# Performance work log

Measured on AMD Instinct MI355X. Metric: run time of the kernel, lower is better.

The kernel has to match this reference:

```python
import jax, jax.numpy as jnp
import numpy as np

B, CIN, IMG, PATCH = 4, 1, 64, 8
SIDE = IMG // PATCH            # 8
N = SIDE ** 3                  # 512 tokens
C = 384
HEADS, HD = 6, 64
IFF = 1536
WS, SHIFT = 2, 1
NB = 4                         # 4 dense blocks + 4 shifted-window blocks (8 layers)
NKP = 15
EPS = 1e-5


def _ln(x, g, b):
    m = x.mean(-1, keepdims=True)
    v = ((x - m) ** 2).mean(-1, keepdims=True)
    return (x - m) * jax.lax.rsqrt(v + EPS) * g + b


def _mhsa(x, qw, kw, vw, pw, pb):
    # per-head Q/K/V linears (no bias), stacked as [H, C, HD]
    q = jnp.einsum('bnc,hcd->bhnd', x, qw)
    k = jnp.einsum('bnc,hcd->bhnd', x, kw)
    v = jnp.einsum('bnc,hcd->bhnd', x, vw)
    a = jax.nn.softmax(jnp.einsum('bhnd,bhmd->bhnm', q, k) / np.float32(np.sqrt(HD)), axis=-1)
    o = jnp.einsum('bhnm,bhmd->bhnd', a, v)
    o = o.transpose(0, 2, 1, 3).reshape(x.shape[0], x.shape[1], C)
    return o @ pw + pb


def _swin_attn(x, qkv_w, qkv_b, pw, pb):
    Bn = x.shape[0]
    H = W = D = SIDE
    xv = x.transpose(0, 2, 1).reshape(Bn, C, H, W, D)
    xv = jnp.roll(xv, (-SHIFT, -SHIFT, -SHIFT), axis=(2, 3, 4))
    # window partition -> [Bn*nw^3, WS^3, C]
    xv = xv.reshape(Bn, C, H // WS, WS, W // WS, WS, D // WS, WS)
    win = xv.transpose(0, 2, 4, 6, 3, 5, 7, 1).reshape(-1, WS ** 3, C)
    qkv = win @ qkv_w + qkv_b                                      # [Bw, ws3, 3C]
    qkv = qkv.reshape(win.shape[0], WS ** 3, 3, HEADS, HD).transpose(2, 0, 3, 1, 4)
    q, k, v = qkv[0], qkv[1], qkv[2]
    a = jax.nn.softmax(jnp.einsum('whnd,whmd->whnm', q, k) / np.float32(np.sqrt(HD)), axis=-1)
    o = jnp.einsum('whnm,whmd->whnd', a, v)
    o = o.transpose(0, 2, 1, 3).reshape(win.shape[0], WS ** 3, C)
    o = o @ pw + pb
    # window reverse
    o = o.reshape(Bn, H // WS, W // WS, D // WS, WS, WS, WS, C)
    o = o.transpose(0, 7, 1, 4, 2, 5, 3, 6).reshape(Bn, C, H, W, D)
    o = jnp.roll(o, (SHIFT, SHIFT, SHIFT), axis=(2, 3, 4))
    return o.reshape(Bn, C, -1).transpose(0, 2, 1)


def _ffn(x, w1, b1, w2, b2):
    return jax.nn.relu(x @ w1 + b1) @ w2 + b2


def _deconv2(x, w, b):
    # ConvTranspose3d kernel=stride=2 (no overlap): pure block upsample GEMM
    Bn, Cc, H, W, D = x.shape
    O = w.shape[1]
    y = jnp.einsum('bchwd,coijk->bohiwjdk', x, w)
    return y.reshape(Bn, O, 2 * H, 2 * W, 2 * D) + b[None, :, None, None, None]


def _bn_relu(x, g, b, m, v):
    sh = (1, -1, 1, 1, 1)
    y = (x - m.reshape(sh)) * jax.lax.rsqrt(v.reshape(sh) + EPS) * g.reshape(sh) + b.reshape(sh)
    return jax.nn.relu(y)


def setup_inputs() -> dict:
    key = jax.random.key(0)
    ks = iter(jax.random.split(key, 40))
    nrm = lambda shape, s=0.02: jax.random.normal(next(ks), shape, jnp.float32) * s
    inp = {
        'x': jax.random.normal(next(ks), (B, CIN, IMG, IMG, IMG), jnp.float32),
        'patch_w': nrm((C, CIN, PATCH, PATCH, PATCH)),
        'patch_b': jnp.zeros((C,), jnp.float32),
        'pos_emb': nrm((1, N, C)),
        # 4 dense blocks (stacked)
        'm_ln1_g': jnp.ones((NB, C)), 'm_ln1_b': jnp.zeros((NB, C)),
        'm_qw': nrm((NB, HEADS, C, HD)), 'm_kw': nrm((NB, HEADS, C, HD)), 'm_vw': nrm((NB, HEADS, C, HD)),
        'm_proj_w': nrm((NB, C, C)), 'm_proj_b': jnp.zeros((NB, C)),
        'm_ln2_g': jnp.ones((NB, C)), 'm_ln2_b': jnp.zeros((NB, C)),
        'm_w1': nrm((NB, C, IFF)), 'm_b1': jnp.zeros((NB, IFF)),
        'm_w2': nrm((NB, IFF, C)), 'm_b2': jnp.zeros((NB, C)),
        # 4 shifted-window blocks (stacked)
        's_ln1_g': jnp.ones((NB, C)), 's_ln1_b': jnp.zeros((NB, C)),
        's_qkv_w': nrm((NB, C, 3 * C)), 's_qkv_b': jnp.zeros((NB, 3 * C)),
        's_proj_w': nrm((NB, C, C)), 's_proj_b': jnp.zeros((NB, C)),
        's_ln2_g': jnp.ones((NB, C)), 's_ln2_b': jnp.zeros((NB, C)),
        's_w1': nrm((NB, C, IFF)), 's_b1': jnp.zeros((NB, IFF)),
        's_w2': nrm((NB, IFF, C)), 's_b2': jnp.zeros((NB, C)),
        # ClassicDecoder
        'd1_w': nrm((C, C, 2, 2, 2)), 'd1_b': jnp.zeros((C,)),
        'bn1_g': jnp.ones((C,)), 'bn1_b': jnp.zeros((C,)), 'bn1_m': jnp.zeros((C,)), 'bn1_v': jnp.ones((C,)),
        'd2_w': nrm((C, C, 2, 2, 2)), 'd2_b': jnp.zeros((C,)),
        'bn2_g': jnp.ones((C,)), 'bn2_b': jnp.zeros((C,)), 'bn2_m': jnp.zeros((C,)), 'bn2_v': jnp.ones((C,)),
        'out_w': nrm((NKP, C)), 'out_b': jnp.zeros((NKP,)),
    }
    return inp


def reference(x, patch_w, patch_b, pos_emb,
              m_ln1_g, m_ln1_b, m_qw, m_kw, m_vw, m_proj_w, m_proj_b,
              m_ln2_g, m_ln2_b, m_w1, m_b1, m_w2, m_b2,
              s_ln1_g, s_ln1_b, s_qkv_w, s_qkv_b, s_proj_w, s_proj_b,
              s_ln2_g, s_ln2_b, s_w1, s_b1, s_w2, s_b2,
              d1_w, d1_b, bn1_g, bn1_b, bn1_m, bn1_v,
              d2_w, d2_b, bn2_g, bn2_b, bn2_m, bn2_v,
              out_w, out_b):
    # patch embedding: Conv3d(k=stride=patch) -> [B, N, C]
    t = jax.lax.conv_general_dilated(x, patch_w, (PATCH, PATCH, PATCH), 'VALID',
                                     dimension_numbers=('NCDHW', 'OIDHW', 'NCDHW'))
    t = t + patch_b[None, :, None, None, None]
    t = t.reshape(B, C, N).transpose(0, 2, 1) + pos_emb
    for i in range(2 * NB):
        j = i // 2
        if i % 2 == 0:  # dense Block
            t = t + _mhsa(_ln(t, m_ln1_g[j], m_ln1_b[j]), m_qw[j], m_kw[j], m_vw[j], m_proj_w[j], m_proj_b[j])
            t = t + _ffn(_ln(t, m_ln2_g[j], m_ln2_b[j]), m_w1[j], m_b1[j], m_w2[j], m_b2[j])
        else:           # ShiftedWindowBlock
            t = t + _swin_attn(_ln(t, s_ln1_g[j], s_ln1_b[j]), s_qkv_w[j], s_qkv_b[j], s_proj_w[j], s_proj_b[j])
            t = t + _ffn(_ln(t, s_ln2_g[j], s_ln2_b[j]), s_w1[j], s_b1[j], s_w2[j], s_b2[j])
    # ClassicDecoder
    y = t.transpose(0, 2, 1).reshape(B, C, SIDE, SIDE, SIDE)
    y = _bn_relu(_deconv2(y, d1_w, d1_b), bn1_g, bn1_b, bn1_m, bn1_v)
    y = _bn_relu(_deconv2(y, d2_w, d2_b), bn2_g, bn2_b, bn2_m, bn2_v)
    y = jnp.einsum('bchwd,oc->bohwd', y, out_w) + out_b[None, :, None, None, None]
    return y
```

## Files before the change

### kernel.cpp

```cpp
#include <hip/hip_runtime.h>
#include <hip/hip_bf16.h>


typedef unsigned short u16;
typedef __bf16 bf16x8 __attribute__((ext_vector_type(8)));
typedef unsigned short u16x8 __attribute__((ext_vector_type(8)));
typedef float f32x4 __attribute__((ext_vector_type(4)));

__device__ __forceinline__ u16 f2bf(float f) {
  unsigned u = __builtin_bit_cast(unsigned, f);
  return (u16)((u + 0x7FFFu + ((u >> 16) & 1u)) >> 16);
}
__device__ __forceinline__ float bf2f(u16 b) {
  unsigned u = ((unsigned)b) << 16;
  return __builtin_bit_cast(float, u);
}

#define GLOAD_LDS16(g, l)                                                      \
  __builtin_amdgcn_global_load_lds(                                            \
      (const __attribute__((address_space(1))) unsigned int*)(const void*)(g), \
      (__attribute__((address_space(3))) unsigned int*)(void*)(l), 16, 0, 0)

struct MmP {
  const u16* A;
  const u16* Bt;
  const float* bias;
  void* C;
  void* aux;
  const float* e1; const float* e2; const float* e3; const float* e4;
  int K, ZH, lda, ldb, ldc;
  long aSb, aSh, bSb, bSh, cSb, cSh;
};

template<int MODE, int BM>
__global__ __launch_bounds__(256) void mfma_gemm(MmP p) {
  const int z = blockIdx.z;
  const int zb = z / p.ZH, zh = z - zb * p.ZH;
  const u16* A  = p.A  + zb * p.aSb + zh * p.aSh;
  const u16* Bt = p.Bt + zb * p.bSb + zh * p.bSh;
  const int m0 = blockIdx.y * BM, n0 = blockIdx.x * 64;

  __shared__ u16 As[2][BM * 64];
  __shared__ u16 Bs[2][64 * 64];

  const int tid = threadIdx.x;
  const int wid = tid >> 6, lane = tid & 63;
  constexpr int MI = BM / 32;
  const int wm = (wid >> 1) * (BM / 2), wn = (wid & 1) * 32;
  const int lr = lane & 15, lg = lane >> 4;
  constexpr int ACH = BM / 32;

  f32x4 acc[MI][2];
  #pragma unroll
  for (int i = 0; i < MI; i++)
    #pragma unroll
    for (int j = 0; j < 2; j++) acc[i][j] = (f32x4){0.f, 0.f, 0.f, 0.f};

  auto stage = [&](int buf, int kt) {
    #pragma unroll
    for (int i = 0; i < ACH; i++) {
      int c = i * 256 + tid;
      int row = c >> 3, cc = c & 7;
      int gk = ((cc ^ (row & 7)) << 3) + (kt << 6);
      GLOAD_LDS16(A + (long)(m0 + row) * p.lda + gk, As[buf] + c * 8);
    }
    #pragma unroll
    for (int i = 0; i < 2; i++) {
      int c = i * 256 + tid;
      int row = c >> 3, cc = c & 7;
      int gk = ((cc ^ (row & 7)) << 3) + (kt << 6);
      GLOAD_LDS16(Bt + (long)(n0 + row) * p.ldb + gk, Bs[buf] + c * 8);
    }
  };

  const int nKT = p.K >> 6;
  stage(0, 0);
  asm volatile("s_waitcnt vmcnt(0)");
  __syncthreads();

  int cur = 0;
  for (int kt = 0; kt < nKT; ++kt) {
    const bool more = (kt + 1 < nKT);
    if (more) stage(cur ^ 1, kt + 1);

    bf16x8 af[MI][2], bfr[2][2];
    #pragma unroll
    for (int i = 0; i < MI; i++)
      #pragma unroll
      for (int ks = 0; ks < 2; ks++) {
        int row = wm + i * 16 + lr;
        int j = ks * 4 + lg;
        af[i][ks] = *(const bf16x8*)(As[cur] + (row * 8 + (j ^ (row & 7))) * 8);
      }
    #pragma unroll
    for (int jn = 0; jn < 2; jn++)
      #pragma unroll
      for (int ks = 0; ks < 2; ks++) {
        int row = wn + jn * 16 + lr;
        int j = ks * 4 + lg;
        bfr[jn][ks] = *(const bf16x8*)(Bs[cur] + (row * 8 + (j ^ (row & 7))) * 8);
      }
    #pragma unroll
    for (int i = 0; i < MI; i++)
      #pragma unroll
      for (int jn = 0; jn < 2; jn++)
        #pragma unroll
        for (int ks = 0; ks < 2; ks++)
          acc[i][jn] = __builtin_amdgcn_mfma_f32_16x16x32_bf16(
              af[i][ks], bfr[jn][ks], acc[i][jn], 0, 0, 0);

    if (more) {
      asm volatile("s_waitcnt vmcnt(0)");
      __syncthreads();
      cur ^= 1;
    }
  }

  const long coff = zb * p.cSb + zh * p.cSh;
  #pragma unroll
  for (int i = 0; i < MI; i++) {
    const int rowb = m0 + wm + i * 16 + lg * 4;
    #pragma unroll
    for (int jn = 0; jn < 2; jn++) {
      const int col = n0 + wn + jn * 16 + lr;
      const float bv = p.bias ? p.bias[col] : 0.f;
      #pragma unroll
      for (int r = 0; r < 4; r++) {
        const int row = rowb + r;
        const float v = acc[i][jn][r];
        if constexpr (MODE == 0) {
          ((u16*)p.C)[coff + (long)row * p.ldc + col] = f2bf(v + bv);
        } else if constexpr (MODE == 1) {
          ((float*)p.C)[coff + (long)row * p.ldc + col] =
              v + bv + p.e1[(long)(row & 511) * 384 + col];
        } else if constexpr (MODE == 2) {
          ((float*)p.C)[coff + (long)row * p.ldc + col] += v + bv;
        } else if constexpr (MODE == 3) {
          ((u16*)p.C)[coff + (long)row * p.ldc + col] = f2bf(fmaxf(v + bv, 0.f));
        } else if constexpr (MODE == 5) {
          float raw = v + bv;
          float val = fmaxf((raw - p.e3[col]) * rsqrtf(p.e4[col] + 1e-5f) * p.e1[col] + p.e2[col], 0.f);
          int b = row >> 9, hwd = row & 511;
          int h = hwd >> 6, w = (hwd >> 3) & 7, d = hwd & 7;
          int i_ = zh >> 2, j_ = (zh >> 1) & 1, k_ = zh & 1;
          long tokn = (long)b * 4096 + (2 * h + i_) * 256 + (2 * w + j_) * 16 + (2 * d + k_);
          ((u16*)p.C)[tokn * 384 + col] = f2bf(val);
        } else if constexpr (MODE == 7) {
          u16 bv16 = f2bf(v);
          ((u16*)p.C)[coff + (long)row * p.ldc + col] = bv16;
          if (col >= 768) {
            int bb = row >> 9, tt = row & 511;
            int hh = (col - 768) >> 6, dd = col & 63;
            ((u16*)p.aux)[(((long)bb * 6 + hh) << 15) + (dd << 9) + tt] = bv16;
          }
        }
      }
    }
  }
}

__global__ __launch_bounds__(512) void dc2_k(const u16* __restrict__ y1, const u16* __restrict__ wd2,
                                             const float* __restrict__ d2b,
                                             const float* __restrict__ g, const float* __restrict__ bta,
                                             const float* __restrict__ mu, const float* __restrict__ var,
                                             const u16* __restrict__ owT, const float* __restrict__ ob,
                                             float* __restrict__ out) {
  __shared__ char smem[114688];
  u16* As = (u16*)smem;
  u16* Bs = (u16*)(smem + 16384);
  u16* H2 = (u16*)(smem + 16384);

  const int ijk = blockIdx.y;
  const int m0 = blockIdx.x * 64;
  const u16* Bt = wd2 + (long)ijk * 147456;
  const int tid = threadIdx.x;
  const int wid = tid >> 6, lane = tid & 63;
  const int wr = wid >> 2, wc = wid & 3;
  const int lr = lane & 15, lg = lane >> 4;

  f32x4 acc[2][6];
  #pragma unroll
  for (int i = 0; i < 2; i++)
    #pragma unroll
    for (int j = 0; j < 6; j++) acc[i][j] = (f32x4){0.f, 0.f, 0.f, 0.f};

  auto stage = [&](int buf, int kt) {
    {
      int c = tid;
      int row = c >> 3, cc = c & 7;
      int gk = ((cc ^ (row & 7)) << 3) + (kt << 6);
      GLOAD_LDS16(y1 + (long)(m0 + row) * 384 + gk, As + buf * 4096 + c * 8);
    }
    #pragma unroll
    for (int i = 0; i < 6; i++) {
      int c = i * 512 + tid;
      int row = c >> 3, cc = c & 7;
      int gk = ((cc ^ (row & 7)) << 3) + (kt << 6);
      GLOAD_LDS16(Bt + (long)row * 384 + gk, Bs + buf * 24576 + c * 8);
    }
  };
  stage(0, 0);
  asm volatile("s_waitcnt vmcnt(0)");
  __syncthreads();
  int cur = 0;
  for (int kt = 0; kt < 6; ++kt) {
    const bool more = (kt < 5);
    if (more) stage(cur ^ 1, kt + 1);
    bf16x8 af[2][2], bfr[6][2];
    #pragma unroll
    for (int i = 0; i < 2; i++)
      #pragma unroll
      for (int ks = 0; ks < 2; ks++) {
        int row = wr * 32 + i * 16 + lr;
        int j = ks * 4 + lg;
        af[i][ks] = *(const bf16x8*)(As + cur * 4096 + (row * 8 + (j ^ (row & 7))) * 8);
      }
    #pragma unroll
    for (int jn = 0; jn < 6; jn++)
      #pragma unroll
      for (int ks = 0; ks < 2; ks++) {
        int row = wc * 96 + jn * 16 + lr;
        int j = ks * 4 + lg;
        bfr[jn][ks] = *(const bf16x8*)(Bs + cur * 24576 + (row * 8 + (j ^ (row & 7))) * 8);
      }
    #pragma unroll
    for (int i = 0; i < 2; i++)
      #pragma unroll
      for (int jn = 0; jn < 6; jn++)
        #pragma unroll
        for (int ks = 0; ks < 2; ks++)
          acc[i][jn] = __builtin_amdgcn_mfma_f32_16x16x32_bf16(
              af[i][ks], bfr[jn][ks], acc[i][jn], 0, 0, 0);
    if (more) {
      asm volatile("s_waitcnt vmcnt(0)");
      __syncthreads();
      cur ^= 1;
    }
  }
  __syncthreads();

  #pragma unroll
  for (int i = 0; i < 2; i++)
    #pragma unroll
    for (int jn = 0; jn < 6; jn++) {
      const int col = wc * 96 + jn * 16 + lr;
      const float scale = rsqrtf(var[col] + 1e-5f) * g[col];
      const float bias2 = bta[col] - mu[col] * scale;
      const float db = d2b[col];
      #pragma unroll
      for (int r = 0; r < 4; r++) {
        int row = wr * 32 + i * 16 + lg * 4 + r;
        float val = fmaxf((acc[i][jn][r] + db) * scale + bias2, 0.f);
        H2[row * 392 + col] = f2bf(val);
      }
    }
  __syncthreads();

  if (wid < 4) {
    f32x4 c4 = (f32x4){0.f, 0.f, 0.f, 0.f};
    #pragma unroll
    for (int mf = 0; mf < 12; mf++) {
      bf16x8 af = *(const bf16x8*)(H2 + (wid * 16 + lr) * 392 + mf * 32 + lg * 8);
      bf16x8 bf = *(const bf16x8*)(owT + lr * 384 + mf * 32 + lg * 8);
      c4 = __builtin_amdgcn_mfma_f32_16x16x32_bf16(af, bf, c4, 0, 0, 0);
    }
    if (lr < 15) {
      const int i_ = ijk >> 2, j_ = (ijk >> 1) & 1, k_ = ijk & 1;
      const float bkp = ob[lr];
      #pragma unroll
      for (int r = 0; r < 4; r++) {
        const int gm = m0 + wid * 16 + lg * 4 + r;
        const int b = gm >> 12, h = (gm >> 8) & 15, w = (gm >> 4) & 15, d = gm & 15;
        const long o = ((long)(b * 15 + lr) << 15) + (2 * h + i_) * 1024 + (2 * w + j_) * 32 + (2 * d + k_);
        out[o] = c4[r] + bkp;
      }
    }
  }
}

__global__ __launch_bounds__(256) void attnsm_k(const u16* __restrict__ qkv, u16* __restrict__ P) {
  const int bh = blockIdx.y;
  const int b = bh / 6, h = bh - b * 6;
  const int qt = blockIdx.x;
  const int tid = threadIdx.x, wid = tid >> 6, lane = tid & 63;
  const int lr = lane & 15, lg = lane >> 4;
  __shared__ u16 Ks[512 * 64];
  const u16* qbase = qkv + ((long)b * 512) * 1152 + h * 64;

  #pragma unroll
  for (int i = 0; i < 16; i++) {
    int c = i * 256 + tid;
    int t = c >> 3, cc = c & 7;
    int gk = (cc ^ (t & 7)) << 3;
    GLOAD_LDS16(qbase + (long)t * 1152 + 384 + gk, Ks + c * 8);
  }
  const int qrow = qt * 64 + wid * 16 + lr;
  bf16x8 qf[2];
  #pragma unroll
  for (int ks = 0; ks < 2; ks++)
    qf[ks] = *(const bf16x8*)(qbase + (long)qrow * 1152 + (ks * 4 + lg) * 8);
  asm volatile("s_waitcnt vmcnt(0)");
  __syncthreads();

  f32x4 s[32];
  #pragma unroll
  for (int nt = 0; nt < 32; nt++) {
    s[nt] = (f32x4){0.f, 0.f, 0.f, 0.f};
    #pragma unroll
    for (int ks = 0; ks < 2; ks++) {
      int row = nt * 16 + lr;
      int j = ks * 4 + lg;
      bf16x8 kf = *(const bf16x8*)(Ks + (row * 8 + (j ^ (row & 7))) * 8);
      s[nt] = __builtin_amdgcn_mfma_f32_16x16x32_bf16(qf[ks], kf, s[nt], 0, 0, 0);
    }
  }
  float mx[4] = {-1e30f, -1e30f, -1e30f, -1e30f};
  #pragma unroll
  for (int nt = 0; nt < 32; nt++)
    #pragma unroll
    for (int r = 0; r < 4; r++) { s[nt][r] *= 0.125f; mx[r] = fmaxf(mx[r], s[nt][r]); }
  #pragma unroll
  for (int o = 8; o >= 1; o >>= 1)
    #pragma unroll
    for (int r = 0; r < 4; r++) mx[r] = fmaxf(mx[r], __shfl_xor(mx[r], o));
  float sum[4] = {0.f, 0.f, 0.f, 0.f};
  #pragma unroll
  for (int nt = 0; nt < 32; nt++)
    #pragma unroll
    for (int r = 0; r < 4; r++) { float e = __expf(s[nt][r] - mx[r]); s[nt][r] = e; sum[r] += e; }
  #pragma unroll
  for (int o = 8; o >= 1; o >>= 1)
    #pragma unroll
    for (int r = 0; r < 4; r++) sum[r] += __shfl_xor(sum[r], o);
  float inv[4];
  #pragma unroll
  for (int r = 0; r < 4; r++) inv[r] = 1.f / sum[r];

  u16* Pb = P + (long)bh * 262144;
  const int prow0 = qt * 64 + wid * 16 + lg * 4;
  #pragma unroll
  for (int nt = 0; nt < 32; nt++)
    #pragma unroll
    for (int r = 0; r < 4; r++)
      Pb[(long)(prow0 + r) * 512 + nt * 16 + lr] = f2bf(s[nt][r] * inv[r]);
}


__global__ __launch_bounds__(256) void ln_k(const float* __restrict__ x, const float* __restrict__ g,
                                            const float* __restrict__ b, u16* __restrict__ y) {
  const int row = (blockIdx.x << 2) + (threadIdx.x >> 6);
  const int lane = threadIdx.x & 63;
  const float* xr = x + (long)row * 384;
  float v[6]; float s = 0.f;
  #pragma unroll
  for (int i = 0; i < 6; i++) { v[i] = xr[lane + (i << 6)]; s += v[i]; }
  #pragma unroll
  for (int o = 32; o >= 1; o >>= 1) s += __shfl_xor(s, o);
  const float mean = s * (1.f / 384.f);
  float q = 0.f;
  #pragma unroll
  for (int i = 0; i < 6; i++) { float dd = v[i] - mean; q += dd * dd; }
  #pragma unroll
  for (int o = 32; o >= 1; o >>= 1) q += __shfl_xor(q, o);
  const float rstd = rsqrtf(q * (1.f / 384.f) + 1e-5f);
  u16* yr = y + (long)row * 384;
  #pragma unroll
  for (int i = 0; i < 6; i++) {
    int c = lane + (i << 6);
    yr[c] = f2bf((v[i] - mean) * rstd * g[c] + b[c]);
  }
}

__global__ __launch_bounds__(64) void swin_k(const u16* __restrict__ qkv, u16* __restrict__ attno) {
  const int blk = blockIdx.x;
  const int h = blk % 6; const int bw = blk / 6;
  const int b = bw >> 6, win = bw & 63;
  const int wh = win >> 4, ww = (win >> 2) & 3, wd = win & 3;
  const int lane = threadIdx.x;
  __shared__ float qs[8][68], ks[8][68], vs[8][68], attw[8][8];
  __shared__ int ntok[8];
  if (lane < 8) {
    int i = lane >> 2, j = (lane >> 1) & 1, k = lane & 1;
    int oh = (2 * wh + i + 1) & 7, ow = (2 * ww + j + 1) & 7, od = (2 * wd + k + 1) & 7;
    ntok[lane] = oh * 64 + ow * 8 + od;
  }
  __syncthreads();
  #pragma unroll
  for (int t = 0; t < 8; t++) {
    long base = ((long)b * 512 + ntok[t]) * 1152 + h * 64 + lane;
    qs[t][lane] = bf2f(qkv[base]);
    ks[t][lane] = bf2f(qkv[base + 384]);
    vs[t][lane] = bf2f(qkv[base + 768]);
  }
  __syncthreads();
  const int tq = lane >> 3, tm = lane & 7;
  float sc = 0.f;
  #pragma unroll 16
  for (int d = 0; d < 64; d++) sc += qs[tq][d] * ks[tm][d];
  sc *= 0.125f;
  float mx = sc;
  mx = fmaxf(mx, __shfl_xor(mx, 4));
  mx = fmaxf(mx, __shfl_xor(mx, 2));
  mx = fmaxf(mx, __shfl_xor(mx, 1));
  float e = __expf(sc - mx);
  float sm = e;
  sm += __shfl_xor(sm, 4); sm += __shfl_xor(sm, 2); sm += __shfl_xor(sm, 1);
  attw[tq][tm] = e / sm;
  __syncthreads();
  #pragma unroll
  for (int t = 0; t < 8; t++) {
    float o = 0.f;
    #pragma unroll
    for (int m = 0; m < 8; m++) o += attw[t][m] * vs[m][lane];
    attno[((long)b * 512 + ntok[t]) * 384 + h * 64 + lane] = f2bf(o);
  }
}

__global__ __launch_bounds__(256) void im2col_k(const float* __restrict__ x, u16* __restrict__ xp) {
  const int i = blockIdx.x * 256 + threadIdx.x;
  const int l = i & 511; const int m = i >> 9;
  const int b = m >> 9, n = m & 511;
  const int h = n >> 6, w = (n >> 3) & 7, d = n & 7;
  const int pi = l >> 6, pj = (l >> 3) & 7, pk = l & 7;
  xp[i] = f2bf(x[(long)b * 262144 + (long)(h * 8 + pi) * 4096 + (w * 8 + pj) * 64 + (d * 8 + pk)]);
}

__global__ __launch_bounds__(256) void castw_k(const float* __restrict__ in, u16* __restrict__ out, int n) {
  for (int i = blockIdx.x * 256 + threadIdx.x; i < n; i += gridDim.x * 256)
    out[i] = f2bf(in[i]);
}

__global__ __launch_bounds__(256) void owrep_k(const float* __restrict__ ow, u16* __restrict__ owT) {
  const int i = blockIdx.x * 256 + threadIdx.x;
  if (i < 6144) owT[i] = (i < 5760) ? f2bf(ow[i]) : (u16)0;
}

struct TJ { const float* s[7]; u16* d[7]; };
__global__ __launch_bounds__(256) void transpose_tiled_k(TJ tj) {
  __shared__ u16 tile[64][65];
  const int cumt[8] = {0, 432, 576, 720, 1296, 1872, 2448, 3024};
  const int bi = blockIdx.x;
  int j = 0;
  #pragma unroll
  for (int t = 1; t < 7; t++) if (bi >= cumt[t]) j = t;
  const int li = bi - cumt[j];
  const int Kj = (j >= 5) ? 1536 : 384;
  const int Nj = (j == 0) ? 1152 : ((j == 3 || j == 4) ? 1536 : 384);
  const int tn_cnt = Nj >> 6;
  const int per_z = (Kj >> 6) * tn_cnt;
  const int z = li / per_z;
  int rem = li - z * per_z;
  const int tk = rem / tn_cnt, tn = rem - tk * tn_cnt;
  const float* src = tj.s[j] + (long)z * Kj * Nj;
  u16* dst = tj.d[j] + (long)z * Kj * Nj;
  const int k0 = tk << 6, n0 = tn << 6;
  const int rl = threadIdx.x >> 6, c = threadIdx.x & 63;
  #pragma unroll
  for (int i = 0; i < 16; i++) {
    int r = i * 4 + rl;
    tile[r][c] = f2bf(src[(long)(k0 + r) * Nj + n0 + c]);
  }
  __syncthreads();
  #pragma unroll
  for (int i = 0; i < 16; i++) {
    int n = i * 4 + rl;
    dst[(long)(n0 + n) * Kj + k0 + c] = tile[c][n];
  }
}

__global__ __launch_bounds__(256) void repack_mqkv_k2(const float* __restrict__ qw, const float* __restrict__ kw,
                                                      const float* __restrict__ vw, u16* __restrict__ out) {
  __shared__ u16 tile[64][65];
  const int bi = blockIdx.x;
  const int j = bi / 108;
  int rem = bi - j * 108;
  const int s = rem / 36; rem -= s * 36;
  const int h = rem / 6, tk = rem - h * 6;
  const float* src = (s == 0 ? qw : s == 1 ? kw : vw) + (long)j * 147456;
  const int rl = threadIdx.x >> 6, cc = threadIdx.x & 63;
  #pragma unroll
  for (int i = 0; i < 16; i++) {
    int cl = tk * 64 + i * 4 + rl;
    tile[i * 4 + rl][cc] = f2bf(src[(long)(h * 384 + cl) * 64 + cc]);
  }
  __syncthreads();
  u16* ob = out + (long)j * 442368 + (long)(s * 384 + h * 64) * 384 + tk * 64;
  #pragma unroll
  for (int i = 0; i < 16; i++) {
    int d = i * 4 + rl;
    ob[(long)d * 384 + cc] = tile[cc][d];
  }
}

__global__ __launch_bounds__(256) void repack_dw2_k(const float* __restrict__ in1, u16* __restrict__ out1,
                                                    const float* __restrict__ in2, u16* __restrict__ out2) {
  __shared__ u16 ds[32][514];
  const int sel = blockIdx.x >= 72;
  const float* in = sel ? in2 : in1;
  u16* out = sel ? out2 : out1;
  const int bx = sel ? blockIdx.x - 72 : blockIdx.x;
  const int bo = bx % 6, bc = bx / 6;
  const int c0 = bc * 32, o0 = bo * 64;
  #pragma unroll 4
  for (int it = 0; it < 64; it++) {
    int fl = it * 256 + threadIdx.x;
    int cr = fl >> 9, mm = fl & 511;
    ds[cr][mm] = f2bf(in[(long)(c0 + cr) * 3072 + o0 * 8 + mm]);
  }
  __syncthreads();
  #pragma unroll 4
  for (int it = 0; it < 64; it++) {
    int fl = it * 256 + threadIdx.x;
    int ijk = fl >> 11, rem = fl & 2047;
    int oo = rem >> 5, cr = rem & 31;
    out[(long)ijk * 147456 + (long)(o0 + oo) * 384 + c0 + cr] = ds[cr][oo * 8 + ijk];
  }
}


static MmP mk(const u16* A, const u16* Bt, const float* bias, void* C,
              int K, int lda, int ldb, int ldc) {
  MmP p{};
  p.A = A; p.Bt = Bt; p.bias = bias; p.C = C; p.aux = nullptr;
  p.e1 = p.e2 = p.e3 = p.e4 = nullptr;
  p.K = K; p.ZH = 1; p.lda = lda; p.ldb = ldb; p.ldc = ldc;
  p.aSb = p.aSh = p.bSb = p.bSh = p.cSb = p.cSh = 0;
  return p;
}

extern "C" void kernel_launch(void* const* d_in, const int* in_sizes, int n_in,
                              void* d_out, int out_size, void* d_ws, size_t ws_size,
                              hipStream_t stream) {
  (void)in_sizes; (void)n_in; (void)out_size; (void)ws_size;
  const float* x        = (const float*)d_in[0];
  const float* patch_w  = (const float*)d_in[1];
  const float* patch_b  = (const float*)d_in[2];
  const float* pos_emb  = (const float*)d_in[3];
  const float* m_ln1_g  = (const float*)d_in[4];
  const float* m_ln1_b  = (const float*)d_in[5];
  const float* m_qw     = (const float*)d_in[6];
  const float* m_kw     = (const float*)d_in[7];
  const float* m_vw     = (const float*)d_in[8];
  const float* m_proj_w = (const float*)d_in[9];
  const float* m_proj_b = (const float*)d_in[10];
  const float* m_ln2_g  = (const float*)d_in[11];
  const float* m_ln2_b  = (const float*)d_in[12];
  const float* m_w1     = (const float*)d_in[13];
  const float* m_b1     = (const float*)d_in[14];
  const float* m_w2     = (const float*)d_in[15];
  const float* m_b2     = (const float*)d_in[16];
  const float* s_ln1_g  = (const float*)d_in[17];
  const float* s_ln1_b  = (const float*)d_in[18];
  const float* s_qkv_w  = (const float*)d_in[19];
  const float* s_qkv_b  = (const float*)d_in[20];
  const float* s_proj_w = (const float*)d_in[21];
  const float* s_proj_b = (const float*)d_in[22];
  const float* s_ln2_g  = (const float*)d_in[23];
  const float* s_ln2_b  = (const float*)d_in[24];
  const float* s_w1     = (const float*)d_in[25];
  const float* s_b1     = (const float*)d_in[26];
  const float* s_w2     = (const float*)d_in[27];
  const float* s_b2     = (const float*)d_in[28];
  const float* d1_w     = (const float*)d_in[29];
  const float* d1_b     = (const float*)d_in[30];
  const float* bn1_g    = (const float*)d_in[31];
  const float* bn1_b    = (const float*)d_in[32];
  const float* bn1_m    = (const float*)d_in[33];
  const float* bn1_v    = (const float*)d_in[34];
  const float* d2_w     = (const float*)d_in[35];
  const float* d2_b     = (const float*)d_in[36];
  const float* bn2_g    = (const float*)d_in[37];
  const float* bn2_b    = (const float*)d_in[38];
  const float* bn2_m    = (const float*)d_in[39];
  const float* bn2_v    = (const float*)d_in[40];
  const float* out_w    = (const float*)d_in[41];
  const float* out_b    = (const float*)d_in[42];
  float* out = (float*)d_out;

  char* wsp = (char*)d_ws;
  auto alloc = [&](size_t bytes) { void* p = wsp; wsp += (bytes + 255) & ~(size_t)255; return p; };
  float* tok    = (float*)alloc(786432 * 4);
  u16* wqkv_m   = (u16*)alloc(1769472 * 2);
  u16* wqkv_s   = (u16*)alloc(1769472 * 2);
  u16* wproj_m  = (u16*)alloc(589824 * 2);
  u16* wproj_s  = (u16*)alloc(589824 * 2);
  u16* w1m      = (u16*)alloc(2359296 * 2);
  u16* w1s      = (u16*)alloc(2359296 * 2);
  u16* w2m      = (u16*)alloc(2359296 * 2);
  u16* w2s      = (u16*)alloc(2359296 * 2);
  u16* wpatch   = (u16*)alloc(196608 * 2);
  u16* wd1      = (u16*)alloc(1179648 * 2);
  u16* wd2      = (u16*)alloc(1179648 * 2);
  u16* owT      = (u16*)alloc(6144 * 2);
  u16* lnb      = (u16*)alloc(786432 * 2);
  u16* qkvb     = (u16*)alloc(2359296 * 2);
  u16* attnob   = (u16*)alloc(786432 * 2);
  u16* ffnhb    = (u16*)alloc(3145728 * 2);
  u16* scoresb  = (u16*)alloc(6291456 * 2);
  u16* vTb      = (u16*)alloc(786432 * 2);
  u16* xpb   = scoresb;
  u16* y1b   = scoresb;
  u16* tokb  = vTb;

  castw_k<<<256, 256, 0, stream>>>(patch_w, wpatch, 196608);
  repack_mqkv_k2<<<432, 256, 0, stream>>>(m_qw, m_kw, m_vw, wqkv_m);
  {
    TJ tj;
    tj.s[0] = s_qkv_w;  tj.d[0] = wqkv_s;
    tj.s[1] = m_proj_w; tj.d[1] = wproj_m;
    tj.s[2] = s_proj_w; tj.d[2] = wproj_s;
    tj.s[3] = m_w1;     tj.d[3] = w1m;
    tj.s[4] = s_w1;     tj.d[4] = w1s;
    tj.s[5] = m_w2;     tj.d[5] = w2m;
    tj.s[6] = s_w2;     tj.d[6] = w2s;
    transpose_tiled_k<<<3024, 256, 0, stream>>>(tj);
  }
  repack_dw2_k<<<144, 256, 0, stream>>>(d1_w, wd1, d2_w, wd2);
  owrep_k<<<24, 256, 0, stream>>>(out_w, owT);

  im2col_k<<<4096, 256, 0, stream>>>(x, xpb);
  {
    MmP p = mk(xpb, wpatch, patch_b, tok, 512, 512, 512, 384);
    p.e1 = pos_emb;
    mfma_gemm<1, 64><<<dim3(6, 32, 1), 256, 0, stream>>>(p);
  }

  for (int j = 0; j < 4; j++) {
    ln_k<<<512, 256, 0, stream>>>(tok, m_ln1_g + j * 384, m_ln1_b + j * 384, lnb);
    {
      MmP p = mk(lnb, wqkv_m + (long)j * 442368, nullptr, qkvb, 384, 384, 384, 1152);
      p.aux = vTb;
      mfma_gemm<7, 128><<<dim3(18, 16, 1), 256, 0, stream>>>(p);
    }
    attnsm_k<<<dim3(8, 24, 1), 256, 0, stream>>>(qkvb, scoresb);
    {
      MmP p = mk(scoresb, vTb, nullptr, attnob, 512, 512, 512, 384);
      p.ZH = 6; p.aSb = 1572864; p.aSh = 262144; p.bSb = 196608; p.bSh = 32768;
      p.cSb = 196608; p.cSh = 64;
      mfma_gemm<0, 64><<<dim3(1, 8, 24), 256, 0, stream>>>(p);
    }
    {
      MmP p = mk(attnob, wproj_m + (long)j * 147456, m_proj_b + j * 384, tok, 384, 384, 384, 384);
      mfma_gemm<2, 64><<<dim3(6, 32, 1), 256, 0, stream>>>(p);
    }
    ln_k<<<512, 256, 0, stream>>>(tok, m_ln2_g + j * 384, m_ln2_b + j * 384, lnb);
    {
      MmP p = mk(lnb, w1m + (long)j * 589824, m_b1 + j * 1536, ffnhb, 384, 384, 384, 1536);
      mfma_gemm<3, 128><<<dim3(24, 16, 1), 256, 0, stream>>>(p);
    }
    {
      MmP p = mk(ffnhb, w2m + (long)j * 589824, m_b2 + j * 384, tok, 1536, 1536, 1536, 384);
      mfma_gemm<2, 64><<<dim3(6, 32, 1), 256, 0, stream>>>(p);
    }

    ln_k<<<512, 256, 0, stream>>>(tok, s_ln1_g + j * 384, s_ln1_b + j * 384, lnb);
    {
      MmP p = mk(lnb, wqkv_s + (long)j * 442368, s_qkv_b + j * 1152, qkvb, 384, 384, 384, 1152);
      mfma_gemm<0, 128><<<dim3(18, 16, 1), 256, 0, stream>>>(p);
    }
    swin_k<<<1536, 64, 0, stream>>>(qkvb, attnob);
    {
      MmP p = mk(attnob, wproj_s + (long)j * 147456, s_proj_b + j * 384, tok, 384, 384, 384, 384);
      mfma_gemm<2, 64><<<dim3(6, 32, 1), 256, 0, stream>>>(p);
    }
    ln_k<<<512, 256, 0, stream>>>(tok, s_ln2_g + j * 384, s_ln2_b + j * 384, lnb);
    {
      MmP p = mk(lnb, w1s + (long)j * 589824, s_b1 + j * 1536, ffnhb, 384, 384, 384, 1536);
      mfma_gemm<3, 128><<<dim3(24, 16, 1), 256, 0, stream>>>(p);
    }
    {
      MmP p = mk(ffnhb, w2s + (long)j * 589824, s_b2 + j * 384, tok, 1536, 1536, 1536, 384);
      mfma_gemm<2, 64><<<dim3(6, 32, 1), 256, 0, stream>>>(p);
    }
  }

  castw_k<<<768, 256, 0, stream>>>(tok, tokb, 786432);
  {
    MmP p = mk(tokb, wd1, d1_b, y1b, 384, 384, 384, 384);
    p.ZH = 8; p.bSh = 147456;
    p.e1 = bn1_g; p.e2 = bn1_b; p.e3 = bn1_m; p.e4 = bn1_v;
    mfma_gemm<5, 128><<<dim3(6, 16, 8), 256, 0, stream>>>(p);
  }
  dc2_k<<<dim3(256, 8, 1), 512, 0, stream>>>(y1b, wd2, d2_b, bn2_g, bn2_b, bn2_m, bn2_v,
                                             owT, out_b, out);
}
```

Measured before the change: 878.4 us.

## Loop dc2 kernel over all eight deconv offsets with A tile held in LDS

```diff
diff --git a/kernel.cpp b/kernel.cpp
--- a/kernel.cpp
+++ b/kernel.cpp
@@ -4,7 +4,6 @@
 
 typedef unsigned short u16;
 typedef __bf16 bf16x8 __attribute__((ext_vector_type(8)));
-typedef unsigned short u16x8 __attribute__((ext_vector_type(8)));
 typedef float f32x4 __attribute__((ext_vector_type(4)));
 
 __device__ __forceinline__ u16 f2bf(float f) {
@@ -165,116 +164,126 @@
                                              const float* __restrict__ mu, const float* __restrict__ var,
                                              const u16* __restrict__ owT, const float* __restrict__ ob,
                                              float* __restrict__ out) {
-  __shared__ char smem[114688];
-  u16* As = (u16*)smem;
-  u16* Bs = (u16*)(smem + 16384);
-  u16* H2 = (u16*)(smem + 16384);
-
-  const int ijk = blockIdx.y;
+  __shared__ char smem[147456];
+  u16* Afull = (u16*)smem;
+  u16* Bb = (u16*)(smem + 49152);
+
   const int m0 = blockIdx.x * 64;
-  const u16* Bt = wd2 + (long)ijk * 147456;
   const int tid = threadIdx.x;
   const int wid = tid >> 6, lane = tid & 63;
   const int wr = wid >> 2, wc = wid & 3;
   const int lr = lane & 15, lg = lane >> 4;
 
-  f32x4 acc[2][6];
-  #pragma unroll
-  for (int i = 0; i < 2; i++)
-    #pragma unroll
-    for (int j = 0; j < 6; j++) acc[i][j] = (f32x4){0.f, 0.f, 0.f, 0.f};
-
-  auto stage = [&](int buf, int kt) {
-    {
-      int c = tid;
-      int row = c >> 3, cc = c & 7;
-      int gk = ((cc ^ (row & 7)) << 3) + (kt << 6);
-      GLOAD_LDS16(y1 + (long)(m0 + row) * 384 + gk, As + buf * 4096 + c * 8);
-    }
+  auto stageB = [&](int buf, int ijk, int kt) {
+    const u16* Bt = wd2 + (long)ijk * 147456;
     #pragma unroll
     for (int i = 0; i < 6; i++) {
       int c = i * 512 + tid;
       int row = c >> 3, cc = c & 7;
       int gk = ((cc ^ (row & 7)) << 3) + (kt << 6);
-      GLOAD_LDS16(Bt + (long)row * 384 + gk, Bs + buf * 24576 + c * 8);
+      GLOAD_LDS16(Bt + (long)row * 384 + gk, Bb + buf * 24576 + c * 8);
     }
   };
-  stage(0, 0);
+
+  #pragma unroll
+  for (int i = 0; i < 6; i++) {
+    int c = tid;
+    int row = c >> 3, cc = c & 7;
+    int gk = ((cc ^ (row & 7)) << 3) + (i << 6);
+    GLOAD_LDS16(y1 + (long)(m0 + row) * 384 + gk, Afull + i * 4096 + c * 8);
+  }
+  stageB(0, 0, 0);
   asm volatile("s_waitcnt vmcnt(0)");
   __syncthreads();
+
   int cur = 0;
-  for (int kt = 0; kt < 6; ++kt) {
-    const bool more = (kt < 5);
-    if (more) stage(cur ^ 1, kt + 1);
-    bf16x8 af[2][2], bfr[6][2];
+  for (int ijk = 0; ijk < 8; ++ijk) {
+    f32x4 acc[2][6];
     #pragma unroll
     for (int i = 0; i < 2; i++)
       #pragma unroll
-      for (int ks = 0; ks < 2; ks++) {
-        int row = wr * 32 + i * 16 + lr;
-        int j = ks * 4 + lg;
-        af[i][ks] = *(const bf16x8*)(As + cur * 4096 + (row * 8 + (j ^ (row & 7))) * 8);
-      }
-    #pragma unroll
-    for (int jn = 0; jn < 6; jn++)
-      #pragma unroll
-      for (int ks = 0; ks < 2; ks++) {
-        int row = wc * 96 + jn * 16 + lr;
-        int j = ks * 4 + lg;
-        bfr[jn][ks] = *(const bf16x8*)(Bs + cur * 24576 + (row * 8 + (j ^ (row & 7))) * 8);
-      }
-    #pragma unroll
-    for (int i = 0; i < 2; i++)
+      for (int j = 0; j < 6; j++) acc[i][j] = (f32x4){0.f, 0.f, 0.f, 0.f};
+
+    for (int kt = 0; kt < 6; ++kt) {
+      const bool more = (kt < 5);
+      if (more) stageB(cur ^ 1, ijk, kt + 1);
+      bf16x8 af[2][2], bfr[6][2];
+      #pragma unroll
+      for (int i = 0; i < 2; i++)
+        #pragma unroll
+        for (int ks = 0; ks < 2; ks++) {
+          int row = wr * 32 + i * 16 + lr;
+          int j = ks * 4 + lg;
+          af[i][ks] = *(const bf16x8*)(Afull + kt * 4096 + (row * 8 + (j ^ (row & 7))) * 8);
+        }
       #pragma unroll
       for (int jn = 0; jn < 6; jn++)
         #pragma unroll
-        for (int ks = 0; ks < 2; ks++)
-          acc[i][jn] = __builtin_amdgcn_mfma_f32_16x16x32_bf16(
-              af[i][ks], bfr[jn][ks], acc[i][jn], 0, 0, 0);
-    if (more) {
-      asm volatile("s_waitcnt vmcnt(0)");
-      __syncthreads();
-      cur ^= 1;
-    }
-  }
-  __syncthreads();
-
-  #pragma unroll
-  for (int i = 0; i < 2; i++)
-    #pragma unroll
-    for (int jn = 0; jn < 6; jn++) {
-      const int col = wc * 96 + jn * 16 + lr;
-      const float scale = rsqrtf(var[col] + 1e-5f) * g[col];
-      const float bias2 = bta[col] - mu[col] * scale;
-      const float db = d2b[col];
-      #pragma unroll
-      for (int r = 0; r < 4; r++) {
-        int row = wr * 32 + i * 16 + lg * 4 + r;
-        float val = fmaxf((acc[i][jn][r] + db) * scale + bias2, 0.f);
-        H2[row * 392 + col] = f2bf(val);
+        for (int ks = 0; ks < 2; ks++) {
+          int row = wc * 96 + jn * 16 + lr;
+          int j = ks * 4 + lg;
+          bfr[jn][ks] = *(const bf16x8*)(Bb + cur * 24576 + (row * 8 + (j ^ (row & 7))) * 8);
+        }
+      #pragma unroll
+      for (int i = 0; i < 2; i++)
+        #pragma unroll
+        for (int jn = 0; jn < 6; jn++)
+          #pragma unroll
+          for (int ks = 0; ks < 2; ks++)
+            acc[i][jn] = __builtin_amdgcn_mfma_f32_16x16x32_bf16(
+                af[i][ks], bfr[jn][ks], acc[i][jn], 0, 0, 0);
+      if (more) {
+        asm volatile("s_waitcnt vmcnt(0)");
+        __syncthreads();
+        cur ^= 1;
       }
     }
-  __syncthreads();
-
-  if (wid < 4) {
-    f32x4 c4 = (f32x4){0.f, 0.f, 0.f, 0.f};
-    #pragma unroll
-    for (int mf = 0; mf < 12; mf++) {
-      bf16x8 af = *(const bf16x8*)(H2 + (wid * 16 + lr) * 392 + mf * 32 + lg * 8);
-      bf16x8 bf = *(const bf16x8*)(owT + lr * 384 + mf * 32 + lg * 8);
-      c4 = __builtin_amdgcn_mfma_f32_16x16x32_bf16(af, bf, c4, 0, 0, 0);
-    }
-    if (lr < 15) {
-      const int i_ = ijk >> 2, j_ = (ijk >> 1) & 1, k_ = ijk & 1;
-      const float bkp = ob[lr];
-      #pragma unroll
-      for (int r = 0; r < 4; r++) {
-        const int gm = m0 + wid * 16 + lg * 4 + r;
-        const int b = gm >> 12, h = (gm >> 8) & 15, w = (gm >> 4) & 15, d = gm & 15;
-        const long o = ((long)(b * 15 + lr) << 15) + (2 * h + i_) * 1024 + (2 * w + j_) * 32 + (2 * d + k_);
-        out[o] = c4[r] + bkp;
+    __syncthreads();
+
+    u16* hbuf = Bb + (cur ^ 1) * 24576;
+    #pragma unroll
+    for (int i = 0; i < 2; i++)
+      #pragma unroll
+      for (int jn = 0; jn < 6; jn++) {
+        const int col = wc * 96 + jn * 16 + lr;
+        const int cc = col >> 3, e = col & 7;
+        const float scale = rsqrtf(var[col] + 1e-5f) * g[col];
+        const float bias2 = bta[col] - mu[col] * scale;
+        const float db = d2b[col];
+        #pragma unroll
+        for (int r = 0; r < 4; r++) {
+          int row = wr * 32 + i * 16 + lg * 4 + r;
+          float val = fmaxf((acc[i][jn][r] + db) * scale + bias2, 0.f);
+          hbuf[row * 384 + ((cc ^ (row & 7)) << 3) + e] = f2bf(val);
+        }
       }
-    }
+    if (ijk < 7) stageB(cur, ijk + 1, 0);
+    __syncthreads();
+
+    if (wid < 4) {
+      f32x4 c4 = (f32x4){0.f, 0.f, 0.f, 0.f};
+      const int row = wid * 16 + lr;
+      #pragma unroll
+      for (int mf = 0; mf < 12; mf++) {
+        int j = mf * 4 + lg;
+        bf16x8 af = *(const bf16x8*)(hbuf + row * 384 + ((j ^ (row & 7)) << 3));
+        bf16x8 bf = *(const bf16x8*)(owT + lr * 384 + j * 8);
+        c4 = __builtin_amdgcn_mfma_f32_16x16x32_bf16(af, bf, c4, 0, 0, 0);
+      }
+      if (lr < 15) {
+        const int i_ = ijk >> 2, j_ = (ijk >> 1) & 1, k_ = ijk & 1;
+        const float bkp = ob[lr];
+        #pragma unroll
+        for (int r = 0; r < 4; r++) {
+          const int gm = m0 + wid * 16 + lg * 4 + r;
+          const int b = gm >> 12, h = (gm >> 8) & 15, w = (gm >> 4) & 15, d = gm & 15;
+          const long o = ((long)(b * 15 + lr) << 15) + (2 * h + i_) * 1024 + (2 * w + j_) * 32 + (2 * d + k_);
+          out[o] = c4[r] + bkp;
+        }
+      }
+    }
+    if (ijk < 7) asm volatile("s_waitcnt vmcnt(0)");
+    __syncthreads();
   }
 }
 
@@ -430,11 +439,6 @@
     out[i] = f2bf(in[i]);
 }
 
-__global__ __launch_bounds__(256) void owrep_k(const float* __restrict__ ow, u16* __restrict__ owT) {
-  const int i = blockIdx.x * 256 + threadIdx.x;
-  if (i < 6144) owT[i] = (i < 5760) ? f2bf(ow[i]) : (u16)0;
-}
-
 struct TJ { const float* s[7]; u16* d[7]; };
 __global__ __launch_bounds__(256) void transpose_tiled_k(TJ tj) {
   __shared__ u16 tile[64][65];
@@ -493,7 +497,13 @@
 }
 
 __global__ __launch_bounds__(256) void repack_dw2_k(const float* __restrict__ in1, u16* __restrict__ out1,
-                                                    const float* __restrict__ in2, u16* __restrict__ out2) {
+                                                    const float* __restrict__ in2, u16* __restrict__ out2,
+                                                    const float* __restrict__ ow, u16* __restrict__ owT) {
+  if (blockIdx.x >= 144) {
+    for (int i = threadIdx.x; i < 6144; i += 256)
+      owT[i] = (i < 5760) ? f2bf(ow[i]) : (u16)0;
+    return;
+  }
   __shared__ u16 ds[32][514];
   const int sel = blockIdx.x >= 72;
   const float* in = sel ? in2 : in1;
@@ -615,8 +625,7 @@
     tj.s[6] = s_w2;     tj.d[6] = w2s;
     transpose_tiled_k<<<3024, 256, 0, stream>>>(tj);
   }
-  repack_dw2_k<<<144, 256, 0, stream>>>(d1_w, wd1, d2_w, wd2);
-  owrep_k<<<24, 256, 0, stream>>>(out_w, owT);
+  repack_dw2_k<<<145, 256, 0, stream>>>(d1_w, wd1, d2_w, wd2, out_w, owT);
 
   im2col_k<<<4096, 256, 0, stream>>>(x, xpb);
   {
@@ -681,6 +690,6 @@
     p.e1 = bn1_g; p.e2 = bn1_b; p.e3 = bn1_m; p.e4 = bn1_v;
     mfma_gemm<5, 128><<<dim3(6, 16, 8), 256, 0, stream>>>(p);
   }
-  dc2_k<<<dim3(256, 8, 1), 512, 0, stream>>>(y1b, wd2, d2_b, bn2_g, bn2_b, bn2_m, bn2_v,
-                                             owT, out_b, out);
-}
+  dc2_k<<<256, 512, 0, stream>>>(y1b, wd2, d2_b, bn2_g, bn2_b, bn2_m, bn2_v,
+                                 owT, out_b, out);
+}
```

Result: slower. 897.6 us (+2.2%).
